# Performance work log

Hardware: AMD Instinct MI355X
Metric: run time of the kernel (lower is better)

## Reference

```python
import jax, jax.numpy as jnp
import numpy as np

NPOINT = 1024
RADIUS = 0.4
NSAMPLE = 32
BN_EPS = 1e-3  # keras BatchNormalization default epsilon


def _fps(xyz, npoint):
    # xyz: [N,3] -> indices [npoint] via farthest point sampling (seed index 0)
    N = xyz.shape[0]

    def step(carry, _):
        dists, far = carry
        d = jnp.sum((xyz - xyz[far]) ** 2, axis=-1)
        dists = jnp.minimum(dists, d)
        return (dists, jnp.argmax(dists).astype(jnp.int32)), far

    init = (jnp.full((N,), 1e10, dtype=xyz.dtype), jnp.asarray(0, dtype=jnp.int32))
    _, idx = jax.lax.scan(step, init, None, length=npoint)
    return idx


def _ball_query(xyz, new_xyz, radius, nsample):
    # xyz: [N,3], new_xyz: [S,3] -> idx [S,nsample]
    # First up-to-nsample points (in original index order) within radius of each
    # center; slots past the count are filled with the first found index
    # (matching the CUDA query_ball_point semantics).
    N = xyz.shape[0]
    d2 = jnp.sum((new_xyz[:, None, :] - xyz[None, :, :]) ** 2, axis=-1)  # [S,N]
    key = jnp.where(d2 < radius * radius, jnp.arange(N, dtype=jnp.int32), N)
    sk = jnp.sort(key, axis=-1)[:, :nsample]          # first valid indices, padded with N
    first = sk[:, :1]
    first = jnp.where(first < N, first, 0)            # fallback if no neighbor found
    idx = jnp.where(sk < N, sk, first)
    return idx.astype(jnp.int32)


def _gather(pts, idx):
    # pts: [B,N,C], idx: [B,...] -> [B,...,C]
    return jax.vmap(lambda p, i: p[i])(pts, idx)


def _conv_bn_relu(x, W, b, g, be):
    # 1x1 conv over [B,P,S,Cin] + batchnorm (training mode, batch stats) + relu
    y = jnp.einsum('bpsc,co->bpso', x, W) + b
    m = jnp.mean(y, axis=(0, 1, 2))
    v = jnp.var(y, axis=(0, 1, 2))
    y = (y - m) * jax.lax.rsqrt(v + BN_EPS) * g + be
    return jax.nn.relu(y)


def setup_inputs() -> dict:
    key = jax.random.key(0)
    ks = jax.random.split(key, 8)
    B, N, C = 16, 4096, 64
    xyz = jax.random.normal(ks[0], (B, N, 3), dtype=jnp.float32)
    points = jax.random.normal(ks[1], (B, N, C), dtype=jnp.float32)
    chans = [3 + C, 64, 64, 128]
    inp = {'xyz': xyz, 'points': points}
    for i in range(3):
        cin, cout = chans[i], chans[i + 1]
        limit = np.sqrt(6.0 / (cin + cout))  # glorot uniform
        inp[f'W{i}'] = jax.random.uniform(ks[2 + i], (cin, cout), jnp.float32, -limit, limit)
        inp[f'b{i}'] = jnp.zeros((cout,), jnp.float32)
        inp[f'g{i}'] = jnp.ones((cout,), jnp.float32)
        inp[f'be{i}'] = jnp.zeros((cout,), jnp.float32)
    return inp


def reference(xyz, points, W0, b0, g0, be0, W1, b1, g1, be1, W2, b2, g2, be2):
    xyz_c = jax.lax.stop_gradient(xyz)
    fps_idx = jax.vmap(lambda p: _fps(p, NPOINT))(xyz_c)           # [B,NPOINT]
    new_xyz = _gather(xyz, fps_idx)                                 # [B,NPOINT,3]
    idx = jax.vmap(lambda p, c: _ball_query(p, c, RADIUS, NSAMPLE))(
        xyz_c, jax.lax.stop_gradient(new_xyz))                      # [B,NPOINT,NSAMPLE]
    grouped_xyz = _gather(xyz, idx) - new_xyz[:, :, None, :]        # centered local coords
    grouped_points = _gather(points, idx)                           # [B,NPOINT,NSAMPLE,C]
    new_points = jnp.concatenate([grouped_xyz, grouped_points], axis=-1)
    new_points = _conv_bn_relu(new_points, W0, b0, g0, be0)
    new_points = _conv_bn_relu(new_points, W1, b1, g1, be1)
    new_points = _conv_bn_relu(new_points, W2, b2, g2, be2)
    new_points = jnp.max(new_points, axis=2)                        # max-pool over nsample
    return (new_xyz, new_points, idx)
```

## Files before the change

kernel.cpp:

```cpp
#include <hip/hip_runtime.h>

static constexpr int NB      = 16;
static constexpr int NPTS    = 4096;
static constexpr int NPOINTS = 1024;
static constexpr int NSAMP   = 32;
static constexpr int CIN0    = 67;
static constexpr int C0      = 64;
static constexpr int C1      = 64;
static constexpr int C2      = 128;
static constexpr size_t MROWS = (size_t)NB * NPOINTS * NSAMP;
#define RAD2 0.16f
#define BN_EPS 0.001f

__device__ __forceinline__ float4 uld4(const float* __restrict__ p) {
    return *(const float4* __restrict__)p;
}

__device__ __forceinline__ unsigned short f2bf(float f) {
    const unsigned u = __float_as_uint(f);
    return (unsigned short)((u + 0x7fffu + ((u >> 16) & 1u)) >> 16);
}
__device__ __forceinline__ float bf2f(unsigned short h) {
    return __uint_as_float((unsigned)h << 16);
}

typedef short bf16x8 __attribute__((ext_vector_type(8)));
typedef float f32x16 __attribute__((ext_vector_type(16)));
union UB { uint4 u; bf16x8 h; };

template<int CTRL>
__device__ __forceinline__ float dppf(float v) {
    return __int_as_float(__builtin_amdgcn_update_dpp(0, __float_as_int(v),
                                                      CTRL, 0xF, 0xF, false));
}
template<int CTRL>
__device__ __forceinline__ float dpps(float v) {
    return __int_as_float(__builtin_amdgcn_update_dpp(__float_as_int(v), __float_as_int(v),
                                                      CTRL, 0xF, 0xF, false));
}
__device__ __forceinline__ float dpp_sum64(float v) {
    v += dppf<0x111>(v); v += dppf<0x112>(v); v += dppf<0x114>(v); v += dppf<0x118>(v);
    v += dppf<0x142>(v); v += dppf<0x143>(v);
    return v;
}
__device__ __forceinline__ float dpp_psum16(float v) {
    v += dppf<0x111>(v); v += dppf<0x112>(v); v += dppf<0x114>(v); v += dppf<0x118>(v);
    return v;
}
__device__ __forceinline__ float dpp_max32(float v) {
    v = fmaxf(v, dpps<0x111>(v)); v = fmaxf(v, dpps<0x112>(v));
    v = fmaxf(v, dpps<0x114>(v)); v = fmaxf(v, dpps<0x118>(v));
    v = fmaxf(v, dpps<0x142>(v));
    return v;
}
__device__ __forceinline__ float dpp_min32(float v) {
    v = fminf(v, dpps<0x111>(v)); v = fminf(v, dpps<0x112>(v));
    v = fminf(v, dpps<0x114>(v)); v = fminf(v, dpps<0x118>(v));
    v = fminf(v, dpps<0x142>(v));
    return v;
}
template<int CTRL>
__device__ __forceinline__ void kstep(unsigned long long& k) {
    const unsigned hi = (unsigned)(k >> 32);
    const unsigned lo = (unsigned)(k & 0xffffffffull);
    const unsigned ohi = (unsigned)__builtin_amdgcn_update_dpp((int)hi, (int)hi, CTRL, 0xF, 0xF, false);
    const unsigned olo = (unsigned)__builtin_amdgcn_update_dpp((int)lo, (int)lo, CTRL, 0xF, 0xF, false);
    const unsigned long long ok = ((unsigned long long)ohi << 32) | olo;
    if (ok > k) k = ok;
}

__global__ __launch_bounds__(512) void fps_kernel(const float* __restrict__ xyz,
                                                  float* __restrict__ out_newxyz,
                                                  float* __restrict__ wsz,
                                                  const float* __restrict__ points,
                                                  const float* __restrict__ W0,
                                                  float* __restrict__ P,
                                                  const float* __restrict__ W2,
                                                  unsigned short* __restrict__ W2t)
{
    if (blockIdx.x == NB) {
        for (int i = threadIdx.x; i < 1024; i += 512) wsz[i] = 0.f;
        if (W2t) {
            for (int i = threadIdx.x; i < C2 * C1; i += 512) {
                const int n = i >> 6, k = i & 63;
                W2t[i] = f2bf(W2[(size_t)k * C2 + n]);
            }
        }
        return;
    }
    if (blockIdx.x > NB) {
        const int r = (blockIdx.x - NB - 1) * 512 + threadIdx.x;
        const float4* pr = (const float4*)(points + (size_t)r * 64);
        float x[64];
#pragma unroll
        for (int j = 0; j < 16; ++j) {
            const float4 v = pr[j];
            x[4*j+0] = v.x; x[4*j+1] = v.y; x[4*j+2] = v.z; x[4*j+3] = v.w;
        }
        float acc[64];
#pragma unroll
        for (int o = 0; o < 64; ++o) acc[o] = 0.f;
#pragma unroll 2
        for (int k = 0; k < 64; ++k) {
            const float xk = x[k];
#pragma unroll
            for (int oc = 0; oc < 16; ++oc) {
                const float4 w4 = uld4(W0 + (3 + k) * 64 + 4 * oc);
                acc[4*oc+0] = fmaf(xk, w4.x, acc[4*oc+0]);
                acc[4*oc+1] = fmaf(xk, w4.y, acc[4*oc+1]);
                acc[4*oc+2] = fmaf(xk, w4.z, acc[4*oc+2]);
                acc[4*oc+3] = fmaf(xk, w4.w, acc[4*oc+3]);
            }
        }
        float4* po = (float4*)(P + (size_t)r * 64);
#pragma unroll
        for (int oc = 0; oc < 16; ++oc)
            po[oc] = make_float4(acc[4*oc+0], acc[4*oc+1], acc[4*oc+2], acc[4*oc+3]);
        return;
    }

    __shared__ float sx[NPTS], sy[NPTS], sz[NPTS];
    __shared__ int   sidx[NPOINTS];
    __shared__ __align__(16) unsigned long long redk[2][8];

    const int b    = blockIdx.x;
    const int tid  = threadIdx.x;
    const int lane = tid & 63;
    const int wv   = tid >> 6;

    const float* base = xyz + (size_t)b * NPTS * 3;
    for (int i = tid; i < NPTS; i += 512) {
        sx[i] = base[i * 3 + 0];
        sy[i] = base[i * 3 + 1];
        sz[i] = base[i * 3 + 2];
    }
    __syncthreads();

    float px[8], py[8], pz[8], dd[8];
#pragma unroll
    for (int j = 0; j < 8; ++j) {
        const int i = tid + j * 512;
        px[j] = sx[i]; py[j] = sy[i]; pz[j] = sz[i];
        dd[j] = 1e10f;
    }

    int   far = 0;
    float fx = sx[0], fy = sy[0], fz = sz[0];
#pragma unroll 1
    for (int it = 0; it < NPOINTS; ++it) {
        if (tid == 0) sidx[it] = far;
        float bv = -1.0f; int bi = 0;
#pragma unroll
        for (int j = 0; j < 8; ++j) {
            const float dx = __fsub_rn(px[j], fx);
            const float dy = __fsub_rn(py[j], fy);
            const float dz = __fsub_rn(pz[j], fz);
            const float d  = __fadd_rn(__fadd_rn(__fmul_rn(dx, dx), __fmul_rn(dy, dy)),
                                       __fmul_rn(dz, dz));
            dd[j] = fminf(dd[j], d);
            if (dd[j] > bv) { bv = dd[j]; bi = tid + j * 512; }
        }
        unsigned long long k = ((unsigned long long)__float_as_uint(bv) << 32)
                             | (unsigned)(4095 - bi);
        kstep<0x111>(k);
        kstep<0x112>(k);
        kstep<0x114>(k);
        kstep<0x118>(k);
        kstep<0x142>(k);
        kstep<0x143>(k);

        const int pb = it & 1;
        if (lane == 63) redk[pb][wv] = k;
        __syncthreads();
        unsigned long long ck = redk[pb][0];
#pragma unroll
        for (int w = 1; w < 8; ++w) {
            const unsigned long long ok = redk[pb][w];
            if (ok > ck) ck = ok;
        }
        const int ci = 4095 - (int)(unsigned)(ck & 0xffffffffull);
        far = ci;
        fx = sx[ci]; fy = sy[ci]; fz = sz[ci];
    }
    __syncthreads();
    for (int it = tid; it < NPOINTS; it += 512) {
        const int ii = sidx[it];
        float* o = out_newxyz + ((size_t)b * NPOINTS + it) * 3;
        o[0] = sx[ii]; o[1] = sy[ii]; o[2] = sz[ii];
    }
}

__global__ __launch_bounds__(256) void ball_kernel(const float* __restrict__ xyz,
                                                   const float* __restrict__ newxyz,
                                                   float* __restrict__ out_idx_f)
{
    __shared__ int sel[4][NSAMP];
    const int tid  = threadIdx.x;
    const int lane = tid & 63;
    const int widx = tid >> 6;
    const int w = blockIdx.x * 4 + widx;
    const int b = w >> 10;

    const float cx = newxyz[(size_t)w * 3 + 0];
    const float cy = newxyz[(size_t)w * 3 + 1];
    const float cz = newxyz[(size_t)w * 3 + 2];
    const float* base = xyz + (size_t)b * NPTS * 3;

    int total = 0;
    for (int c = 0; c < NPTS / 64 && total < NSAMP; ++c) {
        const int n = c * 64 + lane;
        const float dx = __fsub_rn(cx, base[n * 3 + 0]);
        const float dy = __fsub_rn(cy, base[n * 3 + 1]);
        const float dz = __fsub_rn(cz, base[n * 3 + 2]);
        const float d2 = __fadd_rn(__fadd_rn(__fmul_rn(dx, dx), __fmul_rn(dy, dy)),
                                   __fmul_rn(dz, dz));
        const bool pred = d2 < RAD2;
        const unsigned long long mask = __ballot(pred);
        if (pred) {
            const int pos = total + (int)__popcll(mask & ((1ull << lane) - 1ull));
            if (pos < NSAMP) sel[widx][pos] = n;
        }
        total += (int)__popcll(mask);
    }
    __syncthreads();
    if (lane < NSAMP) {
        const int first = sel[widx][0];
        const int v = (lane < total) ? sel[widx][lane] : first;
        out_idx_f[(size_t)w * NSAMP + lane] = (float)v;
    }
}

__device__ __forceinline__ void stats4q(float a0, float a1, float a2, float a3,
                                        float* sa, bool wr)
{
    float q0 = a0*a0, q1 = a1*a1, q2 = a2*a2, q3 = a3*a3;
    a0 = dpp_psum16(a0); q0 = dpp_psum16(q0);
    a1 = dpp_psum16(a1); q1 = dpp_psum16(q1);
    a2 = dpp_psum16(a2); q2 = dpp_psum16(q2);
    a3 = dpp_psum16(a3); q3 = dpp_psum16(q3);
    if (wr) {
        sa[0] += a0; sa[1] += q0; sa[2] += a1; sa[3] += q1;
        sa[4] += a2; sa[5] += q2; sa[6] += a3; sa[7] += q3;
    }
}

__device__ __forceinline__ void stats4(float a0, float a1, float a2, float a3,
                                       float* sa, int lane)
{
    float q0 = a0*a0, q1 = a1*a1, q2 = a2*a2, q3 = a3*a3;
    a0 = dpp_sum64(a0); q0 = dpp_sum64(q0);
    a1 = dpp_sum64(a1); q1 = dpp_sum64(q1);
    a2 = dpp_sum64(a2); q2 = dpp_sum64(q2);
    a3 = dpp_sum64(a3); q3 = dpp_sum64(q3);
    if (lane == 63) {
        sa[0] += a0; sa[1] += q0; sa[2] += a1; sa[3] += q1;
        sa[4] += a2; sa[5] += q2; sa[6] += a3; sa[7] += q3;
    }
}

__device__ __forceinline__ void layer0_dedup(
    const float* __restrict__ xyz, const float* __restrict__ P,
    const float* __restrict__ newxyz, const float* __restrict__ idxf,
    const float* __restrict__ W0, const float* __restrict__ b0,
    int r, float* x1)
{
    const int i  = (int)idxf[r];
    const int bb = r >> 15;
    const int pp = (r >> 5) & 1023;
    const float* pz = xyz + ((size_t)bb * NPTS + i) * 3;
    const float* nz = newxyz + ((size_t)bb * NPOINTS + pp) * 3;
    const float r0 = pz[0] - nz[0];
    const float r1 = pz[1] - nz[1];
    const float r2 = pz[2] - nz[2];
    const float4* prow = (const float4*)(P + ((size_t)bb * NPTS + i) * 64);
#pragma unroll
    for (int oc = 0; oc < 16; ++oc) {
        const float4 pv = prow[oc];
        const float4 bv = uld4(b0 + 4 * oc);
        const float4 wa = uld4(W0 + 0 * 64 + 4 * oc);
        const float4 wb = uld4(W0 + 1 * 64 + 4 * oc);
        const float4 wc = uld4(W0 + 2 * 64 + 4 * oc);
        x1[4*oc+0] = fmaf(r0, wa.x, fmaf(r1, wb.x, fmaf(r2, wc.x, bv.x + pv.x)));
        x1[4*oc+1] = fmaf(r0, wa.y, fmaf(r1, wb.y, fmaf(r2, wc.y, bv.y + pv.y)));
        x1[4*oc+2] = fmaf(r0, wa.z, fmaf(r1, wb.z, fmaf(r2, wc.z, bv.z + pv.z)));
        x1[4*oc+3] = fmaf(r0, wa.w, fmaf(r1, wb.w, fmaf(r2, wc.w, bv.w + pv.w)));
    }
}

__global__ __launch_bounds__(256, 4) void pass0_kernel(
    const float* __restrict__ xyz, const float* __restrict__ P,
    const float* __restrict__ newxyz, const float* __restrict__ idxf,
    const float* __restrict__ W0, const float* __restrict__ b0,
    float* __restrict__ gstats)
{
    __shared__ float sacc[16][2 * C0];
    const int tid  = threadIdx.x;
    const int lane = tid & 63;
    const int wv   = tid >> 6;
    const int slot = wv * 4 + (lane >> 4);
    const bool wr  = (lane & 15) == 15;

    for (int j = tid; j < 16 * 2 * C0; j += 256) (&sacc[0][0])[j] = 0.f;
    __syncthreads();

    const int r = blockIdx.x * 256 + tid;
    float x1[C0];
    layer0_dedup(xyz, P, newxyz, idxf, W0, b0, r, x1);

#pragma unroll
    for (int oc = 0; oc < 16; ++oc)
        stats4q(x1[4*oc+0], x1[4*oc+1], x1[4*oc+2], x1[4*oc+3], &sacc[slot][8*oc], wr);

    __syncthreads();
    for (int j = tid; j < 2 * C0; j += 256) {
        float s = 0.f;
#pragma unroll
        for (int q = 0; q < 16; ++q) s += sacc[q][j];
        atomicAdd(&gstats[j], s);
    }
}

__global__ __launch_bounds__(256, 3) void pass1Y_kernel(
    const float* __restrict__ xyz, const float* __restrict__ P,
    const float* __restrict__ newxyz, const float* __restrict__ idxf,
    const float* __restrict__ W0, const float* __restrict__ b0,
    const float* __restrict__ W1, const float* __restrict__ b1,
    const float* __restrict__ ss0,
    float* __restrict__ gstats, unsigned short* __restrict__ y1b)
{
    __shared__ float sacc[16][2 * C0];
    const int tid  = threadIdx.x;
    const int lane = tid & 63;
    const int wv   = tid >> 6;
    const int slot = wv * 4 + (lane >> 4);
    const bool wr  = (lane & 15) == 15;

    for (int j = tid; j < 16 * 2 * C0; j += 256) (&sacc[0][0])[j] = 0.f;
    __syncthreads();

    const int r = blockIdx.x * 256 + tid;
    float x1[C0];
    layer0_dedup(xyz, P, newxyz, idxf, W0, b0, r, x1);
#pragma unroll
    for (int o = 0; o < C0; ++o)
        x1[o] = fmaxf(0.f, fmaf(x1[o], ss0[o], ss0[64 + o]));

    float y1[C1];
#pragma unroll
    for (int o = 0; o < C1; o += 4) {
        const float4 bv = uld4(b1 + o);
        y1[o] = bv.x; y1[o+1] = bv.y; y1[o+2] = bv.z; y1[o+3] = bv.w;
    }
#pragma unroll 2
    for (int k = 0; k < C0; ++k) {
        const float xk = x1[k];
#pragma unroll
        for (int oc = 0; oc < 16; ++oc) {
            const float4 w4 = uld4(W1 + k * 64 + 4 * oc);
            y1[4*oc+0] = fmaf(xk, w4.x, y1[4*oc+0]);
            y1[4*oc+1] = fmaf(xk, w4.y, y1[4*oc+1]);
            y1[4*oc+2] = fmaf(xk, w4.z, y1[4*oc+2]);
            y1[4*oc+3] = fmaf(xk, w4.w, y1[4*oc+3]);
        }
    }

#pragma unroll
    for (int oc = 0; oc < 16; ++oc)
        stats4q(y1[4*oc+0], y1[4*oc+1], y1[4*oc+2], y1[4*oc+3], &sacc[slot][8*oc], wr);

    uint4* yo = (uint4*)(y1b + (size_t)r * 64);
#pragma unroll
    for (int gq = 0; gq < 8; ++gq) {
        union { unsigned short u[8]; uint4 v; } pk;
#pragma unroll
        for (int e = 0; e < 8; ++e) pk.u[e] = f2bf(y1[8*gq+e]);
        yo[gq] = pk.v;
    }

    __syncthreads();
    for (int j = tid; j < 2 * C0; j += 256) {
        float s = 0.f;
#pragma unroll
        for (int q = 0; q < 16; ++q) s += sacc[q][j];
        atomicAdd(&gstats[j], s);
    }
}

__global__ __launch_bounds__(256, 3) void p2Ym_kernel(
    const unsigned short* __restrict__ y1b,
    const unsigned short* __restrict__ W2t,
    const float* __restrict__ b2,
    const float* __restrict__ ss1,
    float* __restrict__ gstats, float2* __restrict__ mnmx)
{
    __shared__ float  ssl[2 * C1];
    __shared__ float2 sacc[8][C2];
    __shared__ float2 mnacc[8][C2];

    const int tid  = threadIdx.x;
    const int lane = tid & 63;
    const int w    = tid >> 6;
    const int half = lane >> 5;
    const int col  = lane & 31;
    const int slot = w * 2 + half;

    for (int j = tid; j < 2 * C1; j += 256) ssl[j] = ss1[j];
    __syncthreads();

    const int r = blockIdx.x * 128 + w * 32 + col;

    UB afrag[4];
#pragma unroll
    for (int t = 0; t < 4; ++t) {
        const int ko = t * 16 + half * 8;
        uint4 ua = *(const uint4*)(y1b + (size_t)r * 64 + ko);
        float scs[8], shs[8];
        *(float4*)&scs[0] = *(const float4*)&ssl[ko];
        *(float4*)&scs[4] = *(const float4*)&ssl[ko + 4];
        *(float4*)&shs[0] = *(const float4*)&ssl[64 + ko];
        *(float4*)&shs[4] = *(const float4*)&ssl[64 + ko + 4];
        const unsigned* ud = (const unsigned*)&ua;
        uint4 outw;
        unsigned* od = (unsigned*)&outw;
#pragma unroll
        for (int d = 0; d < 4; ++d) {
            const float flo = bf2f((unsigned short)(ud[d] & 0xffffu));
            const float fhi = bf2f((unsigned short)(ud[d] >> 16));
            const float vlo = fmaxf(0.f, fmaf(flo, scs[2*d],   shs[2*d]));
            const float vhi = fmaxf(0.f, fmaf(fhi, scs[2*d+1], shs[2*d+1]));
            od[d] = ((unsigned)f2bf(vhi) << 16) | (unsigned)f2bf(vlo);
        }
        afrag[t].u = outw;
    }

#pragma unroll
    for (int ct = 0; ct < 4; ++ct) {
        const float bias = b2[ct * 32 + col];
        f32x16 acc;
#pragma unroll
        for (int i = 0; i < 16; ++i) acc[i] = bias;
#pragma unroll
        for (int t = 0; t < 4; ++t) {
            UB bfrag;
            bfrag.u = *(const uint4*)(W2t + (size_t)(ct * 32 + col) * 64 + t * 16 + half * 8);
            acc = __builtin_amdgcn_mfma_f32_32x32x16_bf16(afrag[t].h, bfrag.h, acc, 0, 0, 0);
        }
        float s = 0.f, q = 0.f, mn = 3.4e38f, mx = -3.4e38f;
#pragma unroll
        for (int i = 0; i < 16; ++i) {
            const float v = acc[i];
            s += v; q = fmaf(v, v, q);
            mn = fminf(mn, v); mx = fmaxf(mx, v);
        }
        sacc[slot][ct * 32 + col]  = make_float2(s, q);
        mnacc[slot][ct * 32 + col] = make_float2(mn, mx);
    }

    __syncthreads();
    for (int j = tid; j < C2; j += 256) {
        float s = 0.f, q = 0.f;
#pragma unroll
        for (int v = 0; v < 8; ++v) { s += sacc[v][j].x; q += sacc[v][j].y; }
        atomicAdd(&gstats[2*j], s);
        atomicAdd(&gstats[2*j+1], q);
    }
    for (int j = tid; j < 4 * C2; j += 256) {
        const int wg = j >> 7, ch = j & 127;
        const float2 a = mnacc[2*wg][ch], bq = mnacc[2*wg+1][ch];
        mnmx[((size_t)blockIdx.x * 4 + wg) * C2 + ch] =
            make_float2(fminf(a.x, bq.x), fmaxf(a.y, bq.y));
    }
}

__global__ __launch_bounds__(256) void finY_kernel(const float2* __restrict__ mnmx,
                                                   const float* __restrict__ gs2,
                                                   const float* __restrict__ g2,
                                                   const float* __restrict__ be2,
                                                   float* __restrict__ out_np)
{
    const int t = blockIdx.x * 256 + threadIdx.x;
    const int g = t >> 7;
    const int o = t & 127;
    const float inv  = 1.0f / (float)MROWS;
    const float mean = gs2[2*o] * inv;
    const float var  = fmaxf(0.f, gs2[2*o+1] * inv - mean * mean);
    const float sc   = g2[o] / sqrtf(var + BN_EPS);
    const float sh   = fmaf(-mean, sc, be2[o]);
    const float2 mm  = mnmx[(size_t)g * C2 + o];
    const float y    = (sc >= 0.f) ? mm.y : mm.x;
    out_np[t] = fmaxf(0.f, fmaf(y, sc, sh));
}

template<int C>
__global__ void ss_kernel(const float* __restrict__ gs, const float* __restrict__ g,
                          const float* __restrict__ be, float* __restrict__ ss)
{
    const int o = threadIdx.x;
    const float inv  = 1.0f / (float)MROWS;
    const float mean = gs[2*o] * inv;
    const float var  = fmaxf(0.f, gs[2*o+1] * inv - mean * mean);
    const float sc   = g[o] / sqrtf(var + BN_EPS);
    ss[o]     = sc;
    ss[C + o] = fmaf(-mean, sc, be[o]);
}

__global__ __launch_bounds__(256) void preP_kernel(const float* __restrict__ points,
                                                   const float* __restrict__ W0,
                                                   float* __restrict__ P)
{
    const int r = blockIdx.x * 256 + threadIdx.x;
    const float4* pr = (const float4*)(points + (size_t)r * 64);
    float x[64];
#pragma unroll
    for (int j = 0; j < 16; ++j) {
        const float4 v = pr[j];
        x[4*j+0] = v.x; x[4*j+1] = v.y; x[4*j+2] = v.z; x[4*j+3] = v.w;
    }
    float acc[64];
#pragma unroll
    for (int o = 0; o < 64; ++o) acc[o] = 0.f;
#pragma unroll 2
    for (int k = 0; k < 64; ++k) {
        const float xk = x[k];
#pragma unroll
        for (int oc = 0; oc < 16; ++oc) {
            const float4 w4 = uld4(W0 + (3 + k) * 64 + 4 * oc);
            acc[4*oc+0] = fmaf(xk, w4.x, acc[4*oc+0]);
            acc[4*oc+1] = fmaf(xk, w4.y, acc[4*oc+1]);
            acc[4*oc+2] = fmaf(xk, w4.z, acc[4*oc+2]);
            acc[4*oc+3] = fmaf(xk, w4.w, acc[4*oc+3]);
        }
    }
    float4* po = (float4*)(P + (size_t)r * 64);
#pragma unroll
    for (int oc = 0; oc < 16; ++oc)
        po[oc] = make_float4(acc[4*oc+0], acc[4*oc+1], acc[4*oc+2], acc[4*oc+3]);
}

template<int PHASE>
__global__ __launch_bounds__(256, 2) void passP_kernel(
    const float* __restrict__ xyz, const float* __restrict__ P,
    const float* __restrict__ newxyz, const float* __restrict__ idxf,
    const float* __restrict__ W0, const float* __restrict__ b0,
    const float* __restrict__ W1, const float* __restrict__ b1,
    const float* __restrict__ W2, const float* __restrict__ b2,
    const float* __restrict__ ss0, const float* __restrict__ ss1,
    const float* __restrict__ ss2,
    float* __restrict__ gstats, float* __restrict__ out_np)
{
    constexpr int CS = (PHASE == 2) ? C2 : C0;
    __shared__ float sacc[4][2 * CS];

    const int tid  = threadIdx.x;
    const int lane = tid & 63;
    const int wv   = tid >> 6;

    if constexpr (PHASE <= 2) {
        for (int j = tid; j < 8 * CS; j += 256) (&sacc[0][0])[j] = 0.f;
        __syncthreads();
    }

    const int r = blockIdx.x * 256 + tid;
    float x1[C0];
    layer0_dedup(xyz, P, newxyz, idxf, W0, b0, r, x1);

    if constexpr (PHASE == 0) {
#pragma unroll
        for (int oc = 0; oc < 16; ++oc)
            stats4(x1[4*oc+0], x1[4*oc+1], x1[4*oc+2], x1[4*oc+3], &sacc[wv][8*oc], lane);
    } else {
#pragma unroll
        for (int o = 0; o < C0; ++o)
            x1[o] = fmaxf(0.f, fmaf(x1[o], ss0[o], ss0[64 + o]));

        float y1[C1];
#pragma unroll
        for (int o = 0; o < C1; o += 4) {
            const float4 bv = uld4(b1 + o);
            y1[o] = bv.x; y1[o+1] = bv.y; y1[o+2] = bv.z; y1[o+3] = bv.w;
        }
#pragma unroll 2
        for (int k = 0; k < C0; ++k) {
            const float xk = x1[k];
#pragma unroll
            for (int oc = 0; oc < 16; ++oc) {
                const float4 w4 = uld4(W1 + k * 64 + 4 * oc);
                y1[4*oc+0] = fmaf(xk, w4.x, y1[4*oc+0]);
                y1[4*oc+1] = fmaf(xk, w4.y, y1[4*oc+1]);
                y1[4*oc+2] = fmaf(xk, w4.z, y1[4*oc+2]);
                y1[4*oc+3] = fmaf(xk, w4.w, y1[4*oc+3]);
            }
        }

        if constexpr (PHASE == 1) {
#pragma unroll
            for (int oc = 0; oc < 16; ++oc)
                stats4(y1[4*oc+0], y1[4*oc+1], y1[4*oc+2], y1[4*oc+3], &sacc[wv][8*oc], lane);
        } else {
#pragma unroll
            for (int o = 0; o < C1; ++o)
                y1[o] = fmaxf(0.f, fmaf(y1[o], ss1[o], ss1[64 + o]));

            float a2[C2];
#pragma unroll
            for (int o = 0; o < C2; o += 4) {
                const float4 bv = uld4(b2 + o);
                a2[o] = bv.x; a2[o+1] = bv.y; a2[o+2] = bv.z; a2[o+3] = bv.w;
            }
#pragma unroll 2
            for (int k = 0; k < C1; ++k) {
                const float xk = y1[k];
#pragma unroll
                for (int o = 0; o < C2; o += 4) {
                    const float4 w4 = uld4(W2 + k * C2 + o);
                    a2[o+0] = fmaf(xk, w4.x, a2[o+0]);
                    a2[o+1] = fmaf(xk, w4.y, a2[o+1]);
                    a2[o+2] = fmaf(xk, w4.z, a2[o+2]);
                    a2[o+3] = fmaf(xk, w4.w, a2[o+3]);
                }
            }

            if constexpr (PHASE == 2) {
#pragma unroll
                for (int o = 0; o < C2; ++o) {
                    const float s = dpp_sum64(a2[o]);
                    const float q = dpp_sum64(a2[o] * a2[o]);
                    if (lane == 63) { sacc[wv][2*o] += s; sacc[wv][2*o+1] += q; }
                }
            } else {
                const int g = r >> 5;
#pragma unroll
                for (int o = 0; o < C2; ++o) {
                    float v = fmaxf(0.f, fmaf(a2[o], ss2[o], ss2[C2 + o]));
                    v = dpp_max32(v);
                    if (lane == 31 || lane == 63) out_np[(size_t)g * C2 + o] = v;
                }
            }
        }
    }

    if constexpr (PHASE <= 2) {
        __syncthreads();
        for (int j = tid; j < 2 * CS; j += 256)
            atomicAdd(&gstats[j], sacc[0][j] + sacc[1][j] + sacc[2][j] + sacc[3][j]);
    }
}

template<int PHASE>
__global__ __launch_bounds__(128) void pass_kernel(
    const float* __restrict__ xyz, const float* __restrict__ points,
    const float* __restrict__ newxyz, const float* __restrict__ idxf,
    const float* __restrict__ W0, const float* __restrict__ b0,
    const float* __restrict__ W1, const float* __restrict__ b1,
    const float* __restrict__ W2, const float* __restrict__ b2,
    const float* __restrict__ ss0, const float* __restrict__ ss1,
    const float* __restrict__ ss2,
    float* __restrict__ gstats, float* __restrict__ out_np)
{
    constexpr int CS = (PHASE == 2) ? C2 : C0;
    __shared__ float xld[(PHASE >= 1) ? (64 * 128) : 1];
    __shared__ float sacc[2][2 * CS];

    const int tid  = threadIdx.x;
    const int lane = tid & 63;
    const int wv   = tid >> 6;

    if constexpr (PHASE <= 2) {
        for (int j = tid; j < 2 * 2 * CS; j += 128) (&sacc[0][0])[j] = 0.f;
        __syncthreads();
    }

    const int r  = blockIdx.x * 128 + tid;
    const int i  = (int)idxf[r];
    const int bb = r >> 15;
    const int pp = (r >> 5) & 1023;

    float x[CIN0];
    {
        const float* pz = xyz + ((size_t)bb * NPTS + i) * 3;
        const float* nz = newxyz + ((size_t)bb * NPOINTS + pp) * 3;
        x[0] = pz[0] - nz[0];
        x[1] = pz[1] - nz[1];
        x[2] = pz[2] - nz[2];
        const float4* p4 = (const float4*)(points + ((size_t)bb * NPTS + i) * 64);
#pragma unroll
        for (int j = 0; j < 16; ++j) {
            const float4 v = p4[j];
            x[3+4*j+0] = v.x; x[3+4*j+1] = v.y; x[3+4*j+2] = v.z; x[3+4*j+3] = v.w;
        }
    }

#pragma unroll 1
    for (int oc = 0; oc < 16; ++oc) {
        const float4 bv = uld4(b0 + 4*oc);
        float a0 = bv.x, a1 = bv.y, a2 = bv.z, a3 = bv.w;
#pragma unroll
        for (int k = 0; k < CIN0; ++k) {
            const float4 w4 = uld4(W0 + k*64 + 4*oc);
            a0 = fmaf(x[k], w4.x, a0); a1 = fmaf(x[k], w4.y, a1);
            a2 = fmaf(x[k], w4.z, a2); a3 = fmaf(x[k], w4.w, a3);
        }
        if constexpr (PHASE == 0) {
            stats4(a0, a1, a2, a3, &sacc[wv][8*oc], lane);
        } else {
            xld[(4*oc+0)*128 + tid] = fmaxf(0.f, fmaf(a0, ss0[4*oc+0], ss0[64+4*oc+0]));
            xld[(4*oc+1)*128 + tid] = fmaxf(0.f, fmaf(a1, ss0[4*oc+1], ss0[64+4*oc+1]));
            xld[(4*oc+2)*128 + tid] = fmaxf(0.f, fmaf(a2, ss0[4*oc+2], ss0[64+4*oc+2]));
            xld[(4*oc+3)*128 + tid] = fmaxf(0.f, fmaf(a3, ss0[4*oc+3], ss0[64+4*oc+3]));
        }
    }

    if constexpr (PHASE == 1) {
#pragma unroll 1
        for (int oc = 0; oc < 16; ++oc) {
            const float4 bv = uld4(b1 + 4*oc);
            float a0 = bv.x, a1 = bv.y, a2 = bv.z, a3 = bv.w;
#pragma unroll
            for (int k = 0; k < 64; ++k) {
                const float xk = xld[k*128 + tid];
                const float4 w4 = uld4(W1 + k*64 + 4*oc);
                a0 = fmaf(xk, w4.x, a0); a1 = fmaf(xk, w4.y, a1);
                a2 = fmaf(xk, w4.z, a2); a3 = fmaf(xk, w4.w, a3);
            }
            stats4(a0, a1, a2, a3, &sacc[wv][8*oc], lane);
        }
    }

    if constexpr (PHASE >= 2) {
        float acc2[C2];
#pragma unroll
        for (int o = 0; o < C2; o += 4) {
            const float4 bv = uld4(b2 + o);
            acc2[o] = bv.x; acc2[o+1] = bv.y; acc2[o+2] = bv.z; acc2[o+3] = bv.w;
        }
#pragma unroll 1
        for (int oc = 0; oc < 16; ++oc) {
            const float4 bv = uld4(b1 + 4*oc);
            float a0 = bv.x, a1 = bv.y, a2 = bv.z, a3 = bv.w;
#pragma unroll
            for (int k = 0; k < 64; ++k) {
                const float xk = xld[k*128 + tid];
                const float4 w4 = uld4(W1 + k*64 + 4*oc);
                a0 = fmaf(xk, w4.x, a0); a1 = fmaf(xk, w4.y, a1);
                a2 = fmaf(xk, w4.z, a2); a3 = fmaf(xk, w4.w, a3);
            }
            const float xc0 = fmaxf(0.f, fmaf(a0, ss1[4*oc+0], ss1[64+4*oc+0]));
            const float xc1 = fmaxf(0.f, fmaf(a1, ss1[4*oc+1], ss1[64+4*oc+1]));
            const float xc2 = fmaxf(0.f, fmaf(a2, ss1[4*oc+2], ss1[64+4*oc+2]));
            const float xc3 = fmaxf(0.f, fmaf(a3, ss1[4*oc+3], ss1[64+4*oc+3]));
#pragma unroll
            for (int o = 0; o < C2; o += 4) {
                const float4 wA = uld4(W2 + (4*oc+0)*C2 + o);
                const float4 wB = uld4(W2 + (4*oc+1)*C2 + o);
                const float4 wC = uld4(W2 + (4*oc+2)*C2 + o);
                const float4 wD = uld4(W2 + (4*oc+3)*C2 + o);
                acc2[o+0] = fmaf(xc0, wA.x, fmaf(xc1, wB.x, fmaf(xc2, wC.x, fmaf(xc3, wD.x, acc2[o+0]))));
                acc2[o+1] = fmaf(xc0, wA.y, fmaf(xc1, wB.y, fmaf(xc2, wC.y, fmaf(xc3, wD.y, acc2[o+1]))));
                acc2[o+2] = fmaf(xc0, wA.z, fmaf(xc1, wB.z, fmaf(xc2, wC.z, fmaf(xc3, wD.z, acc2[o+2]))));
                acc2[o+3] = fmaf(xc0, wA.w, fmaf(xc1, wB.w, fmaf(xc2, wC.w, fmaf(xc3, wD.w, acc2[o+3]))));
            }
        }

        if constexpr (PHASE == 2) {
#pragma unroll
            for (int o = 0; o < C2; ++o) {
                const float s = dpp_sum64(acc2[o]);
                const float q = dpp_sum64(acc2[o] * acc2[o]);
                if (lane == 63) { sacc[wv][2*o] += s; sacc[wv][2*o+1] += q; }
            }
        } else {
            const int g = r >> 5;
#pragma unroll
            for (int o = 0; o < C2; ++o) {
                float v = fmaxf(0.f, fmaf(acc2[o], ss2[o], ss2[C2+o]));
                v = dpp_max32(v);
                if (lane == 31 || lane == 63) out_np[(size_t)g * C2 + o] = v;
            }
        }
    }

    if constexpr (PHASE <= 2) {
        __syncthreads();
        for (int j = tid; j < 2 * CS; j += 128)
            atomicAdd(&gstats[j], sacc[0][j] + sacc[1][j]);
    }
}

extern "C" void kernel_launch(void* const* d_in, const int* in_sizes, int n_in,
                              void* d_out, int out_size, void* d_ws, size_t ws_size,
                              hipStream_t stream)
{
    (void)in_sizes; (void)n_in; (void)out_size;
    const float* xyz    = (const float*)d_in[0];
    const float* points = (const float*)d_in[1];
    const float* W0  = (const float*)d_in[2];
    const float* b0  = (const float*)d_in[3];
    const float* g0  = (const float*)d_in[4];
    const float* be0 = (const float*)d_in[5];
    const float* W1  = (const float*)d_in[6];
    const float* b1  = (const float*)d_in[7];
    const float* g1  = (const float*)d_in[8];
    const float* be1 = (const float*)d_in[9];
    const float* W2  = (const float*)d_in[10];
    const float* b2  = (const float*)d_in[11];
    const float* g2  = (const float*)d_in[12];
    const float* be2 = (const float*)d_in[13];

    float* out = (float*)d_out;
    float* out_newxyz = out;
    float* out_newpts = out + (size_t)NB * NPOINTS * 3;
    float* out_idx    = out_newpts + (size_t)NB * NPOINTS * C2;

    float* wsf = (float*)d_ws;
    float* gs0 = wsf + 0;
    float* gs1 = wsf + 128;
    float* gs2 = wsf + 256;
    float* ss0 = wsf + 512;
    float* ss1 = wsf + 640;
    float* ss2 = wsf + 768;
    const size_t PBYTES  = (size_t)NB * NPTS * C0 * 4;
    const size_t MMBYTES = (size_t)NB * NPOINTS * 2 * C2 * 4;
    const size_t YBYTES  = MROWS * C1 * 2;
    const size_t TBYTES  = (size_t)C2 * C1 * 2;
    float* P    = (float*)((char*)d_ws + 65536);
    float* mnmx = (float*)((char*)d_ws + 65536 + PBYTES);
    unsigned short* y1b = (unsigned short*)((char*)d_ws + 65536 + PBYTES + MMBYTES);
    unsigned short* W2t = (unsigned short*)((char*)d_ws + 65536 + PBYTES + MMBYTES + YBYTES);

    const bool haveP = ws_size >= (65536 + PBYTES);
    const bool haveY = ws_size >= (65536 + PBYTES + MMBYTES + YBYTES + TBYTES);

    const int frontGrid = NB + 1 + (haveP ? (NB * NPTS / 512) : 0);
    fps_kernel<<<frontGrid, 512, 0, stream>>>(xyz, out_newxyz, wsf, points, W0, P,
                                              W2, haveY ? W2t : nullptr);
    ball_kernel<<<(NB * NPOINTS) / 4, 256, 0, stream>>>(xyz, out_newxyz, out_idx);

    if (haveY) {
        const int grid = (int)(MROWS / 256);
        pass0_kernel<<<grid, 256, 0, stream>>>(xyz, P, out_newxyz, out_idx,
                                               W0, b0, gs0);
        ss_kernel<C0><<<1, C0, 0, stream>>>(gs0, g0, be0, ss0);
        pass1Y_kernel<<<grid, 256, 0, stream>>>(xyz, P, out_newxyz, out_idx,
                                                W0, b0, W1, b1, ss0, gs1, y1b);
        ss_kernel<C1><<<1, C1, 0, stream>>>(gs1, g1, be1, ss1);
        p2Ym_kernel<<<(int)(MROWS / 128), 256, 0, stream>>>(y1b, W2t, b2, ss1,
                                                            gs2, (float2*)mnmx);
        finY_kernel<<<NB * NPOINTS * C2 / 256, 256, 0, stream>>>((const float2*)mnmx,
                                                                 gs2, g2, be2, out_newpts);
    } else if (haveP) {
        const int grid = (int)(MROWS / 256);
        passP_kernel<0><<<grid, 256, 0, stream>>>(xyz, P, out_newxyz, out_idx,
                                                  W0, b0, W1, b1, W2, b2,
                                                  ss0, ss1, ss2, gs0, nullptr);
        ss_kernel<C0><<<1, C0, 0, stream>>>(gs0, g0, be0, ss0);
        passP_kernel<1><<<grid, 256, 0, stream>>>(xyz, P, out_newxyz, out_idx,
                                                  W0, b0, W1, b1, W2, b2,
                                                  ss0, ss1, ss2, gs1, nullptr);
        ss_kernel<C1><<<1, C1, 0, stream>>>(gs1, g1, be1, ss1);
        passP_kernel<2><<<grid, 256, 0, stream>>>(xyz, P, out_newxyz, out_idx,
                                                  W0, b0, W1, b1, W2, b2,
                                                  ss0, ss1, ss2, gs2, nullptr);
        ss_kernel<C2><<<1, C2, 0, stream>>>(gs2, g2, be2, ss2);
        passP_kernel<3><<<grid, 256, 0, stream>>>(xyz, P, out_newxyz, out_idx,
                                                  W0, b0, W1, b1, W2, b2,
                                                  ss0, ss1, ss2, nullptr, out_newpts);
    } else {
        const int grid = (int)(MROWS / 128);
        pass_kernel<0><<<grid, 128, 0, stream>>>(xyz, points, out_newxyz, out_idx,
                                                 W0, b0, W1, b1, W2, b2,
                                                 ss0, ss1, ss2, gs0, nullptr);
        ss_kernel<C0><<<1, C0, 0, stream>>>(gs0, g0, be0, ss0);
        pass_kernel<1><<<grid, 128, 0, stream>>>(xyz, points, out_newxyz, out_idx,
                                                 W0, b0, W1, b1, W2, b2,
                                                 ss0, ss1, ss2, gs1, nullptr);
        ss_kernel<C1><<<1, C1, 0, stream>>>(gs1, g1, be1, ss1);
        pass_kernel<2><<<grid, 128, 0, stream>>>(xyz, points, out_newxyz, out_idx,
                                                 W0, b0, W1, b1, W2, b2,
                                                 ss0, ss1, ss2, gs2, nullptr);
        ss_kernel<C2><<<1, C2, 0, stream>>>(gs2, g2, be2, ss2);
        pass_kernel<3><<<grid, 128, 0, stream>>>(xyz, points, out_newxyz, out_idx,
                                                 W0, b0, W1, b1, W2, b2,
                                                 ss0, ss1, ss2, nullptr, out_newpts);
    }
}
```

Baseline: 1.202 ms.

## Process two batches per FPS block to amortize per-iteration barrier latency

The farthest-point-sampling kernel now handles two point clouds per 512-thread block, interleaving their distance updates, DPP reductions and cross-wave reductions so that both share a single __syncthreads per iteration. This halves the number of FPS blocks and hides the latency-bound serial chain of one batch behind the other's work. In exchange each block uses twice the LDS and registers, and fewer CUs run FPS concurrently. The preP_kernel definition is moved and is also launched on the haveP-only fallback path.

```diff
diff --git a/kernel.cpp b/kernel.cpp
--- a/kernel.cpp
+++ b/kernel.cpp
@@ -8,6 +8,7 @@
 static constexpr int C0      = 64;
 static constexpr int C1      = 64;
 static constexpr int C2      = 128;
+static constexpr int FB      = NB / 2;
 static constexpr size_t MROWS = (size_t)NB * NPOINTS * NSAMP;
 #define RAD2 0.16f
 #define BN_EPS 0.001f
@@ -78,7 +79,7 @@
                                                   const float* __restrict__ W2,
                                                   unsigned short* __restrict__ W2t)
 {
-    if (blockIdx.x == NB) {
+    if (blockIdx.x == FB) {
         for (int i = threadIdx.x; i < 1024; i += 512) wsz[i] = 0.f;
         if (W2t) {
             for (int i = threadIdx.x; i < C2 * C1; i += 512) {
@@ -88,8 +89,8 @@
         }
         return;
     }
-    if (blockIdx.x > NB) {
-        const int r = (blockIdx.x - NB - 1) * 512 + threadIdx.x;
+    if (blockIdx.x > FB) {
+        const int r = (blockIdx.x - FB - 1) * 512 + threadIdx.x;
         const float4* pr = (const float4*)(points + (size_t)r * 64);
         float x[64];
 #pragma unroll
@@ -119,74 +120,100 @@
         return;
     }
 
-    __shared__ float sx[NPTS], sy[NPTS], sz[NPTS];
-    __shared__ int   sidx[NPOINTS];
-    __shared__ __align__(16) unsigned long long redk[2][8];
-
-    const int b    = blockIdx.x;
+    __shared__ float sxA[NPTS], syA[NPTS], szA[NPTS];
+    __shared__ float sxB[NPTS], syB[NPTS], szB[NPTS];
+    __shared__ int   sidxA[NPOINTS], sidxB[NPOINTS];
+    __shared__ __align__(16) unsigned long long redkA[2][8], redkB[2][8];
+
     const int tid  = threadIdx.x;
     const int lane = tid & 63;
     const int wv   = tid >> 6;
-
-    const float* base = xyz + (size_t)b * NPTS * 3;
+    const int bA   = blockIdx.x * 2;
+    const int bB   = bA + 1;
+
+    const float* baseA = xyz + (size_t)bA * NPTS * 3;
+    const float* baseB = xyz + (size_t)bB * NPTS * 3;
     for (int i = tid; i < NPTS; i += 512) {
-        sx[i] = base[i * 3 + 0];
-        sy[i] = base[i * 3 + 1];
-        sz[i] = base[i * 3 + 2];
+        sxA[i] = baseA[i * 3 + 0]; syA[i] = baseA[i * 3 + 1]; szA[i] = baseA[i * 3 + 2];
+        sxB[i] = baseB[i * 3 + 0]; syB[i] = baseB[i * 3 + 1]; szB[i] = baseB[i * 3 + 2];
     }
     __syncthreads();
 
-    float px[8], py[8], pz[8], dd[8];
+    float pxA[8], pyA[8], pzA[8], ddA[8];
+    float pxB[8], pyB[8], pzB[8], ddB[8];
 #pragma unroll
     for (int j = 0; j < 8; ++j) {
         const int i = tid + j * 512;
-        px[j] = sx[i]; py[j] = sy[i]; pz[j] = sz[i];
-        dd[j] = 1e10f;
-    }
-
-    int   far = 0;
-    float fx = sx[0], fy = sy[0], fz = sz[0];
+        pxA[j] = sxA[i]; pyA[j] = syA[i]; pzA[j] = szA[i]; ddA[j] = 1e10f;
+        pxB[j] = sxB[i]; pyB[j] = syB[i]; pzB[j] = szB[i]; ddB[j] = 1e10f;
+    }
+
+    int   farA = 0, farB = 0;
+    float fxA = sxA[0], fyA = syA[0], fzA = szA[0];
+    float fxB = sxB[0], fyB = syB[0], fzB = szB[0];
+
 #pragma unroll 1
     for (int it = 0; it < NPOINTS; ++it) {
-        if (tid == 0) sidx[it] = far;
-        float bv = -1.0f; int bi = 0;
+        if (tid == 0) { sidxA[it] = farA; sidxB[it] = farB; }
+
+        float bvA = -1.0f; int biA = 0;
 #pragma unroll
         for (int j = 0; j < 8; ++j) {
-            const float dx = __fsub_rn(px[j], fx);
-            const float dy = __fsub_rn(py[j], fy);
-            const float dz = __fsub_rn(pz[j], fz);
+            const float dx = __fsub_rn(pxA[j], fxA);
+            const float dy = __fsub_rn(pyA[j], fyA);
+            const float dz = __fsub_rn(pzA[j], fzA);
             const float d  = __fadd_rn(__fadd_rn(__fmul_rn(dx, dx), __fmul_rn(dy, dy)),
                                        __fmul_rn(dz, dz));
-            dd[j] = fminf(dd[j], d);
-            if (dd[j] > bv) { bv = dd[j]; bi = tid + j * 512; }
-        }
-        unsigned long long k = ((unsigned long long)__float_as_uint(bv) << 32)
-                             | (unsigned)(4095 - bi);
-        kstep<0x111>(k);
-        kstep<0x112>(k);
-        kstep<0x114>(k);
-        kstep<0x118>(k);
-        kstep<0x142>(k);
-        kstep<0x143>(k);
+            ddA[j] = fminf(ddA[j], d);
+            if (ddA[j] > bvA) { bvA = ddA[j]; biA = tid + j * 512; }
+        }
+        unsigned long long kA = ((unsigned long long)__float_as_uint(bvA) << 32)
+                              | (unsigned)(4095 - biA);
+        kstep<0x111>(kA); kstep<0x112>(kA); kstep<0x114>(kA);
+        kstep<0x118>(kA); kstep<0x142>(kA); kstep<0x143>(kA);
+
+        float bvB = -1.0f; int biB = 0;
+#pragma unroll
+        for (int j = 0; j < 8; ++j) {
+            const float dx = __fsub_rn(pxB[j], fxB);
+            const float dy = __fsub_rn(pyB[j], fyB);
+            const float dz = __fsub_rn(pzB[j], fzB);
+            const float d  = __fadd_rn(__fadd_rn(__fmul_rn(dx, dx), __fmul_rn(dy, dy)),
+                                       __fmul_rn(dz, dz));
+            ddB[j] = fminf(ddB[j], d);
+            if (ddB[j] > bvB) { bvB = ddB[j]; biB = tid + j * 512; }
+        }
+        unsigned long long kB = ((unsigned long long)__float_as_uint(bvB) << 32)
+                              | (unsigned)(4095 - biB);
+        kstep<0x111>(kB); kstep<0x112>(kB); kstep<0x114>(kB);
+        kstep<0x118>(kB); kstep<0x142>(kB); kstep<0x143>(kB);
 
         const int pb = it & 1;
-        if (lane == 63) redk[pb][wv] = k;
+        if (lane == 63) { redkA[pb][wv] = kA; redkB[pb][wv] = kB; }
         __syncthreads();
-        unsigned long long ck = redk[pb][0];
+
+        unsigned long long ckA = redkA[pb][0];
+        unsigned long long ckB = redkB[pb][0];
 #pragma unroll
         for (int w = 1; w < 8; ++w) {
-            const unsigned long long ok = redk[pb][w];
-            if (ok > ck) ck = ok;
-        }
-        const int ci = 4095 - (int)(unsigned)(ck & 0xffffffffull);
-        far = ci;
-        fx = sx[ci]; fy = sy[ci]; fz = sz[ci];
+            const unsigned long long oA = redkA[pb][w];
+            const unsigned long long oB = redkB[pb][w];
+            if (oA > ckA) ckA = oA;
+            if (oB > ckB) ckB = oB;
+        }
+        const int ciA = 4095 - (int)(unsigned)(ckA & 0xffffffffull);
+        const int ciB = 4095 - (int)(unsigned)(ckB & 0xffffffffull);
+        farA = ciA; fxA = sxA[ciA]; fyA = syA[ciA]; fzA = szA[ciA];
+        farB = ciB; fxB = sxB[ciB]; fyB = syB[ciB]; fzB = szB[ciB];
     }
     __syncthreads();
     for (int it = tid; it < NPOINTS; it += 512) {
-        const int ii = sidx[it];
-        float* o = out_newxyz + ((size_t)b * NPOINTS + it) * 3;
-        o[0] = sx[ii]; o[1] = sy[ii]; o[2] = sz[ii];
+        int ii = sidxA[it];
+        float* o = out_newxyz + ((size_t)bA * NPOINTS + it) * 3;
+        o[0] = sxA[ii]; o[1] = syA[ii]; o[2] = szA[ii];
+        ii = sidxB[it];
+        o = out_newxyz + ((size_t)bB * NPOINTS + it) * 3;
+        o[0] = sxB[ii]; o[1] = syB[ii]; o[2] = szB[ii];
     }
 }
 
@@ -504,39 +531,6 @@
     ss[C + o] = fmaf(-mean, sc, be[o]);
 }
 
-__global__ __launch_bounds__(256) void preP_kernel(const float* __restrict__ points,
-                                                   const float* __restrict__ W0,
-                                                   float* __restrict__ P)
-{
-    const int r = blockIdx.x * 256 + threadIdx.x;
-    const float4* pr = (const float4*)(points + (size_t)r * 64);
-    float x[64];
-#pragma unroll
-    for (int j = 0; j < 16; ++j) {
-        const float4 v = pr[j];
-        x[4*j+0] = v.x; x[4*j+1] = v.y; x[4*j+2] = v.z; x[4*j+3] = v.w;
-    }
-    float acc[64];
-#pragma unroll
-    for (int o = 0; o < 64; ++o) acc[o] = 0.f;
-#pragma unroll 2
-    for (int k = 0; k < 64; ++k) {
-        const float xk = x[k];
-#pragma unroll
-        for (int oc = 0; oc < 16; ++oc) {
-            const float4 w4 = uld4(W0 + (3 + k) * 64 + 4 * oc);
-            acc[4*oc+0] = fmaf(xk, w4.x, acc[4*oc+0]);
-            acc[4*oc+1] = fmaf(xk, w4.y, acc[4*oc+1]);
-            acc[4*oc+2] = fmaf(xk, w4.z, acc[4*oc+2]);
-            acc[4*oc+3] = fmaf(xk, w4.w, acc[4*oc+3]);
-        }
-    }
-    float4* po = (float4*)(P + (size_t)r * 64);
-#pragma unroll
-    for (int oc = 0; oc < 16; ++oc)
-        po[oc] = make_float4(acc[4*oc+0], acc[4*oc+1], acc[4*oc+2], acc[4*oc+3]);
-}
-
 template<int PHASE>
 __global__ __launch_bounds__(256, 2) void passP_kernel(
     const float* __restrict__ xyz, const float* __restrict__ P,
@@ -644,6 +638,39 @@
         for (int j = tid; j < 2 * CS; j += 256)
             atomicAdd(&gstats[j], sacc[0][j] + sacc[1][j] + sacc[2][j] + sacc[3][j]);
     }
+}
+
+__global__ __launch_bounds__(256) void preP_kernel(const float* __restrict__ points,
+                                                   const float* __restrict__ W0,
+                                                   float* __restrict__ P)
+{
+    const int r = blockIdx.x * 256 + threadIdx.x;
+    const float4* pr = (const float4*)(points + (size_t)r * 64);
+    float x[64];
+#pragma unroll
+    for (int j = 0; j < 16; ++j) {
+        const float4 v = pr[j];
+        x[4*j+0] = v.x; x[4*j+1] = v.y; x[4*j+2] = v.z; x[4*j+3] = v.w;
+    }
+    float acc[64];
+#pragma unroll
+    for (int o = 0; o < 64; ++o) acc[o] = 0.f;
+#pragma unroll 2
+    for (int k = 0; k < 64; ++k) {
+        const float xk = x[k];
+#pragma unroll
+        for (int oc = 0; oc < 16; ++oc) {
+            const float4 w4 = uld4(W0 + (3 + k) * 64 + 4 * oc);
+            acc[4*oc+0] = fmaf(xk, w4.x, acc[4*oc+0]);
+            acc[4*oc+1] = fmaf(xk, w4.y, acc[4*oc+1]);
+            acc[4*oc+2] = fmaf(xk, w4.z, acc[4*oc+2]);
+            acc[4*oc+3] = fmaf(xk, w4.w, acc[4*oc+3]);
+        }
+    }
+    float4* po = (float4*)(P + (size_t)r * 64);
+#pragma unroll
+    for (int oc = 0; oc < 16; ++oc)
+        po[oc] = make_float4(acc[4*oc+0], acc[4*oc+1], acc[4*oc+2], acc[4*oc+3]);
 }
 
 template<int PHASE>
@@ -830,7 +857,7 @@
     const bool haveP = ws_size >= (65536 + PBYTES);
     const bool haveY = ws_size >= (65536 + PBYTES + MMBYTES + YBYTES + TBYTES);
 
-    const int frontGrid = NB + 1 + (haveP ? (NB * NPTS / 512) : 0);
+    const int frontGrid = FB + 1 + (haveP ? (NB * NPTS / 512) : 0);
     fps_kernel<<<frontGrid, 512, 0, stream>>>(xyz, out_newxyz, wsf, points, W0, P,
                                               W2, haveY ? W2t : nullptr);
     ball_kernel<<<(NB * NPOINTS) / 4, 256, 0, stream>>>(xyz, out_newxyz, out_idx);
@@ -849,6 +876,7 @@
                                                                  gs2, g2, be2, out_newpts);
     } else if (haveP) {
         const int grid = (int)(MROWS / 256);
+        preP_kernel<<<NB * NPTS / 256, 256, 0, stream>>>(points, W0, P);
         passP_kernel<0><<<grid, 256, 0, stream>>>(xyz, P, out_newxyz, out_idx,
                                                   W0, b0, W1, b1, W2, b2,
                                                   ss0, ss1, ss2, gs0, nullptr);
```

New measurement: 1.730 ms. +44.0%, slower.
